# Optimization experiments

Measured on AMD Instinct MI355X. Metric: run time of the kernel, lower is better.

Reference implementation:

```python
import jax, jax.numpy as jnp
import numpy as np

PI = np.pi

def _rz(t):
    c, s = jnp.cos(t), jnp.sin(t)
    z, o = jnp.zeros_like(t), jnp.ones_like(t)
    return jnp.stack([jnp.stack([c, -s, z]), jnp.stack([s, c, z]), jnp.stack([z, z, o])])

def _ry(t):
    c, s = jnp.cos(t), jnp.sin(t)
    z, o = jnp.zeros_like(t), jnp.ones_like(t)
    return jnp.stack([jnp.stack([c, z, s]), jnp.stack([z, o, z]), jnp.stack([-s, z, c])])

def _zyz_affine(params, translate):
    # params: [6] in [0,1]; returns rotation matrix [3,3] and offset [3]
    phi   = params[0] * 2.0 * PI - PI
    theta = params[1] * 2.0 * PI - PI
    psi   = params[2] * 2.0 * PI - PI
    loc_r = params[3:6] * 2.0 - 1.0 if translate else params[3:6] * 0.0
    rm = (_rz(phi) @ _ry(theta) @ _rz(psi)).T
    c = -rm @ loc_r
    return rm, c

def _trilinear(img, x, y, z):
    # img: [X,Y,Z,C]; x,y,z: [X,Y,Z] normalized coords in [-1,1]
    xl, yl, zl, _ = img.shape
    x = (x + 1.0) * (xl - 1) * 0.5
    y = (y + 1.0) * (yl - 1) * 0.5
    z = (z + 1.0) * (zl - 1) * 0.5
    x0f, y0f, z0f = jnp.floor(x), jnp.floor(y), jnp.floor(z)
    x0 = jnp.clip(x0f.astype(jnp.int32), 0, xl - 1)
    x1 = jnp.clip(x0f.astype(jnp.int32) + 1, 0, xl - 1)
    y0 = jnp.clip(y0f.astype(jnp.int32), 0, yl - 1)
    y1 = jnp.clip(y0f.astype(jnp.int32) + 1, 0, yl - 1)
    z0 = jnp.clip(z0f.astype(jnp.int32), 0, zl - 1)
    z1 = jnp.clip(z0f.astype(jnp.int32) + 1, 0, zl - 1)
    # original computes dx against the *clipped* lower corner
    dx = (x - x0.astype(x.dtype))[..., None]
    dy = (y - y0.astype(y.dtype))[..., None]
    dz = (z - z0.astype(z.dtype))[..., None]
    out = ((1 - dx) * (1 - dy) * (1 - dz) * img[x0, y0, z0]
         + (1 - dx) * (1 - dy) * dz       * img[x0, y0, z1]
         + (1 - dx) * dy       * (1 - dz) * img[x0, y1, z0]
         + (1 - dx) * dy       * dz       * img[x0, y1, z1]
         + dx       * (1 - dy) * (1 - dz) * img[x1, y0, z0]
         + dx       * (1 - dy) * dz       * img[x1, y0, z1]
         + dx       * dy       * (1 - dz) * img[x1, y1, z0]
         + dx       * dy       * dz       * img[x1, y1, z1])
    return out

def _affine_warp(img, rm, c):
    xl, yl, zl = img.shape[:3]
    gx = jnp.linspace(-1.0, 1.0, xl)
    gy = jnp.linspace(-1.0, 1.0, yl)
    gz = jnp.linspace(-1.0, 1.0, zl)
    grids = jnp.stack(jnp.meshgrid(gx, gy, gz, indexing='ij'))  # [3,X,Y,Z]
    tg = jnp.einsum('ij,jxyz->ixyz', rm, grids) + c[:, None, None, None]
    return _trilinear(img, tg[0], tg[1], tg[2])

def _ft3d(x):
    # chain of three 1D FFTs + fftshift over spatial axes == fftshift(fftn)
    return jnp.fft.fftshift(jnp.fft.fftn(x.astype(jnp.complex64), axes=(1, 2, 3)), axes=(1, 2, 3))

def _ift3d(x):
    return jnp.fft.ifftn(jnp.fft.ifftshift(x, axes=(1, 2, 3)), axes=(1, 2, 3))

def setup_inputs() -> dict:
    key = jax.random.key(0)
    ks = jax.random.split(key, 5)
    B, N, C = 32, 64, 1
    return {
        'X': jax.random.normal(ks[0], (B, N, N, N, C), jnp.float32),
        'Y': jax.random.normal(ks[1], (B, N, N, N, C), jnp.float32),
        'm1': jax.random.uniform(ks[2], (B, N, N, N, C), jnp.float32),
        'm2': jax.random.uniform(ks[3], (B, N, N, N, C), jnp.float32),
        'theta': jax.random.uniform(ks[4], (B, 6), jnp.float32),
    }

def reference(X, Y, m1, m2, theta):
    # masks: rotation only (zero translation)
    mask_warp = jax.vmap(lambda m, p: _affine_warp(m, *_zyz_affine(p, False)))
    M1_t = mask_warp(m1, theta)
    M2_t = mask_warp(m2, theta)
    # 'fill' padding: rescale translations by shape/(shape+2), zero-pad, warp, crop
    shape = jnp.asarray(X.shape[1:4], jnp.float32)
    scale = jnp.concatenate([jnp.ones(3, jnp.float32), shape / (shape + 2.0)])
    theta_r = (theta - 0.5) * scale + 0.5
    Xp = jnp.pad(X, ((0, 0), (1, 1), (1, 1), (1, 1), (0, 0)))
    img_warp = jax.vmap(lambda im, p: _affine_warp(im, *_zyz_affine(p, True)))
    X_t = img_warp(Xp, theta_r)[:, 1:-1, 1:-1, 1:-1, :]
    fused = _ft3d(X_t) * M1_t.astype(jnp.complex64) + _ft3d(Y) * M2_t.astype(jnp.complex64)
    output = jnp.real(_ift3d(fused)).astype(jnp.float32)
    return output, M1_t, M2_t
```

## Files before the change

### kernel.cpp

```cpp
#include <hip/hip_runtime.h>
#include <math.h>

#define NB 32
#define NN 4096
#define NNN 262144
#define PERMI(i) ((((i)&7)<<3)|((i)>>3))

__device__ __forceinline__ float2 cadd(float2 a, float2 b){ return make_float2(a.x+b.x, a.y+b.y); }
__device__ __forceinline__ float2 csub(float2 a, float2 b){ return make_float2(a.x-b.x, a.y-b.y); }
__device__ __forceinline__ float2 cmulc(float2 a, float2 b){ return make_float2(a.x*b.x - a.y*b.y, a.x*b.y + a.y*b.x); }
template<int S> __device__ __forceinline__ float2 cmuli(float2 a){
  return (S>0)? make_float2(-a.y,a.x) : make_float2(a.y,-a.x);
}

template<int S>
__device__ __forceinline__ void dft8(float2* a){
  const float r_ = 0.70710678118654752f;
  float2 t0=cadd(a[0],a[4]), t1=csub(a[0],a[4]);
  float2 t2=cadd(a[2],a[6]), t3=csub(a[2],a[6]);
  float2 u0=cadd(a[1],a[5]), u1=csub(a[1],a[5]);
  float2 u2=cadd(a[3],a[7]), u3=csub(a[3],a[7]);
  float2 E0=cadd(t0,t2), E2=csub(t0,t2);
  float2 it3=cmuli<S>(t3);
  float2 E1=cadd(t1,it3), E3=csub(t1,it3);
  float2 O0=cadd(u0,u2), O2=csub(u0,u2);
  float2 iu3=cmuli<S>(u3);
  float2 O1=cadd(u1,iu3), O3=csub(u1,iu3);
  const float sr = (S>0)? r_ : -r_;
  float2 W1 = make_float2(r_, sr);
  float2 W3 = make_float2(-r_, sr);
  float2 o1 = cmulc(O1,W1);
  float2 o2 = cmuli<S>(O2);
  float2 o3 = cmulc(O3,W3);
  a[0]=cadd(E0,O0); a[4]=csub(E0,O0);
  a[1]=cadd(E1,o1); a[5]=csub(E1,o1);
  a[2]=cadd(E2,o2); a[6]=csub(E2,o2);
  a[3]=cadd(E3,o3); a[7]=csub(E3,o3);
}

#define TWTAB \
  const float TWC[8]={1.f,0.9951847266721969f,0.9807852804032304f,0.9569403357322088f, \
                      0.9238795325112867f,0.8819212643483551f,0.8314696123025452f,0.7730104533627370f}; \
  const float TWS[8]={0.f,0.0980171403295606f,0.1950903220161283f,0.2902846772544624f, \
                      0.3826834323650898f,0.4713967368259976f,0.5555702330196022f,0.6343932841636455f};

template<int S>
__device__ __forceinline__ void fft64(float2* v){
  #pragma unroll
  for(int n2=0;n2<8;n2++){
    float2 t[8];
    #pragma unroll
    for(int n1=0;n1<8;n1++) t[n1] = v[8*n1+n2];
    dft8<S>(t);
    #pragma unroll
    for(int k1=0;k1<8;k1++) v[8*k1+n2] = t[k1];
  }
  TWTAB
  #pragma unroll
  for(int k1=1;k1<8;k1++){
    float2 wb = make_float2(TWC[k1], (S>0)? TWS[k1] : -TWS[k1]);
    float2 w = wb;
    #pragma unroll
    for(int n2=1;n2<8;n2++){
      v[8*k1+n2] = cmulc(v[8*k1+n2], w);
      w = cmulc(w, wb);
    }
  }
  #pragma unroll
  for(int k1=0;k1<8;k1++){
    float2 t[8];
    #pragma unroll
    for(int n2=0;n2<8;n2++) t[n2]=v[8*k1+n2];
    dft8<S>(t);
    #pragma unroll
    for(int k2=0;k2<8;k2++) v[8*k1+k2]=t[k2];
  }
}

template<int S>
__device__ __forceinline__ void fft64_pin_nat(float2* v){
  #pragma unroll
  for(int r=0;r<8;r++){
    float2 t[8];
    #pragma unroll
    for(int a=0;a<8;a++) t[a]=v[8*r+a];
    dft8<S>(t);
    #pragma unroll
    for(int q=0;q<8;q++) v[8*r+q]=t[q];
  }
  TWTAB
  #pragma unroll
  for(int r=1;r<8;r++){
    float2 wb = make_float2(TWC[r], (S>0)? TWS[r] : -TWS[r]);
    float2 w = wb;
    #pragma unroll
    for(int q=1;q<8;q++){
      v[8*r+q] = cmulc(v[8*r+q], w);
      w = cmulc(w, wb);
    }
  }
  #pragma unroll
  for(int q=0;q<8;q++){
    float2 t[8];
    #pragma unroll
    for(int b=0;b<8;b++) t[b]=v[8*b+q];
    dft8<S>(t);
    #pragma unroll
    for(int m=0;m<8;m++) v[8*m+q]=t[m];
  }
}

__global__ void k_affine(const float* __restrict__ theta, float* __restrict__ aff){
  int b = threadIdx.x;
  if(b >= NB) return;
  const float* t = theta + b*6;
  const float PIf = 3.14159265358979323846f;
  float phi = t[0]*(2.f*PIf) - PIf;
  float th  = t[1]*(2.f*PIf) - PIf;
  float psi = t[2]*(2.f*PIf) - PIf;
  float cph = cosf(phi), sph = sinf(phi);
  float cth = cosf(th),  sth = sinf(th);
  float cps = cosf(psi), sps = sinf(psi);
  float R00 = cph*cth*cps - sph*sps;
  float R01 = -cph*cth*sps - sph*cps;
  float R02 = cph*sth;
  float R10 = sph*cth*cps + cph*sps;
  float R11 = -sph*cth*sps + cph*cps;
  float R12 = sph*sth;
  float R20 = -sth*cps;
  float R21 = sth*sps;
  float R22 = cth;
  float rm0=R00, rm1=R10, rm2=R20;
  float rm3=R01, rm4=R11, rm5=R21;
  float rm6=R02, rm7=R12, rm8=R22;
  float* o = aff + b*16;
  o[0]=rm0; o[1]=rm1; o[2]=rm2;
  o[3]=rm3; o[4]=rm4; o[5]=rm5;
  o[6]=rm6; o[7]=rm7; o[8]=rm8;
  const float sc = 64.0f/66.0f;
  float lx = (2.f*t[3]-1.f)*sc;
  float ly = (2.f*t[4]-1.f)*sc;
  float lz = (2.f*t[5]-1.f)*sc;
  o[9]  = -(rm0*lx + rm1*ly + rm2*lz);
  o[10] = -(rm3*lx + rm4*ly + rm5*lz);
  o[11] = -(rm6*lx + rm7*ly + rm8*lz);
}

__device__ __forceinline__ void tile_decode(int blk, int& batch, int& ox, int& oy, int& oz){
  int xcd = blk & 7;
  int j = blk >> 3;
  batch = xcd + ((j >> 9) << 3);
  int tile = j & 511;
  oz = (tile & 7) << 3;
  oy = ((tile >> 3) & 7) << 3;
  ox = (tile >> 6) << 3;
}

#define LDSI(xi,yi,zi) ((((xi)*16)+(yi))*17+(zi))

__global__ __launch_bounds__(256) void k_warp_masks(const float* __restrict__ m1, const float* __restrict__ m2,
                             const float* __restrict__ aff,
                             float* __restrict__ M1, float* __restrict__ M2){
  __shared__ float s1[16*16*17];
  __shared__ float s2[16*16*17];
  int batch, ox, oy, oz;
  tile_decode(blockIdx.x, batch, ox, oy, oz);
  const float* a = aff + batch*16;
  float a0=a[0],a1=a[1],a2=a[2],a3=a[3],a4=a[4],a5=a[5],a6=a[6],a7=a[7],a8=a[8];

  float gxl = ox*(2.f/63.f)-1.f, gxh = (ox+7)*(2.f/63.f)-1.f;
  float gyl = oy*(2.f/63.f)-1.f, gyh = (oy+7)*(2.f/63.f)-1.f;
  float gzl = oz*(2.f/63.f)-1.f, gzh = (oz+7)*(2.f/63.f)-1.f;
  #define MM(c,lo,hi) fminf((c)*(lo),(c)*(hi))
  float minx = (1.f + MM(a0,gxl,gxh) + MM(a1,gyl,gyh) + MM(a2,gzl,gzh))*31.5f;
  float miny = (1.f + MM(a3,gxl,gxh) + MM(a4,gyl,gyh) + MM(a5,gzl,gzh))*31.5f;
  float minz = (1.f + MM(a6,gxl,gxh) + MM(a7,gyl,gyh) + MM(a8,gzl,gzh))*31.5f;
  #undef MM
  int sx0 = min(max((int)floorf(minx-0.01f),0),48);
  int sy0 = min(max((int)floorf(miny-0.01f),0),48);
  int sz0 = min(max((int)floorf(minz-0.01f),0),48);

  {
    int zi = threadIdx.x & 15, yi = threadIdx.x >> 4;
    const float* p1 = m1 + (size_t)batch*NNN + ((sy0+yi)<<6) + (sz0+zi);
    const float* p2 = m2 + (size_t)batch*NNN + ((sy0+yi)<<6) + (sz0+zi);
    #pragma unroll
    for(int xi=0;xi<16;xi++){
      s1[LDSI(xi,yi,zi)] = p1[(size_t)(sx0+xi)<<12];
      s2[LDSI(xi,yi,zi)] = p2[(size_t)(sx0+xi)<<12];
    }
  }
  __syncthreads();

  #pragma unroll
  for(int o=0;o<2;o++){
    int v = threadIdx.x + o*256;
    int zo = v & 7, yo = (v>>3)&7, xo = v>>6;
    float gx = (ox+xo)*(2.f/63.f)-1.f;
    float gy = (oy+yo)*(2.f/63.f)-1.f;
    float gz = (oz+zo)*(2.f/63.f)-1.f;
    float px = (a0*gx + a1*gy + a2*gz + 1.f)*31.5f;
    float py = (a3*gx + a4*gy + a5*gz + 1.f)*31.5f;
    float pz = (a6*gx + a7*gy + a8*gz + 1.f)*31.5f;
    int xf=(int)floorf(px), yf=(int)floorf(py), zf=(int)floorf(pz);
    int x0=min(max(xf,0),63), x1=min(max(xf+1,0),63);
    int y0=min(max(yf,0),63), y1=min(max(yf+1,0),63);
    int z0=min(max(zf,0),63), z1=min(max(zf+1,0),63);
    float dx=px-(float)x0, dy=py-(float)y0, dz=pz-(float)z0;
    float ex=1.f-dx, ey=1.f-dy, ez=1.f-dz;
    int lx0=min(max(x0-sx0,0),15), lx1=min(max(x1-sx0,0),15);
    int ly0=min(max(y0-sy0,0),15), ly1=min(max(y1-sy0,0),15);
    int lz0=min(max(z0-sz0,0),15), lz1=min(max(z1-sz0,0),15);
    int xA=lx0*272, xB=lx1*272, yA=ly0*17, yB=ly1*17;
    int i000=xA+yA+lz0, i001=xA+yA+lz1, i010=xA+yB+lz0, i011=xA+yB+lz1;
    int i100=xB+yA+lz0, i101=xB+yA+lz1, i110=xB+yB+lz0, i111=xB+yB+lz1;
    float w000=ex*ey*ez, w001=ex*ey*dz, w010=ex*dy*ez, w011=ex*dy*dz;
    float w100=dx*ey*ez, w101=dx*ey*dz, w110=dx*dy*ez, w111=dx*dy*dz;
    float r1 = w000*s1[i000]+w001*s1[i001]+w010*s1[i010]+w011*s1[i011]
             + w100*s1[i100]+w101*s1[i101]+w110*s1[i110]+w111*s1[i111];
    float r2 = w000*s2[i000]+w001*s2[i001]+w010*s2[i010]+w011*s2[i011]
             + w100*s2[i100]+w101*s2[i101]+w110*s2[i110]+w111*s2[i111];
    size_t oi = (size_t)batch*NNN + ((size_t)(ox+xo)<<12) + ((oy+yo)<<6) + (oz+zo);
    M1[oi] = r1;
    M2[oi] = r2;
  }
}

__global__ __launch_bounds__(256) void k_warp_x(const float* __restrict__ X, const float* __restrict__ aff,
                         float* __restrict__ Xt){
  __shared__ float sX[16*16*17];
  int batch, ox, oy, oz;
  tile_decode(blockIdx.x, batch, ox, oy, oz);
  const float* a = aff + batch*16;
  float a0=a[0],a1=a[1],a2=a[2],a3=a[3],a4=a[4],a5=a[5],a6=a[6],a7=a[7],a8=a[8];
  float c0=a[9], c1=a[10], c2=a[11];

  float gxl = (ox+1)*(2.f/65.f)-1.f, gxh = (ox+8)*(2.f/65.f)-1.f;
  float gyl = (oy+1)*(2.f/65.f)-1.f, gyh = (oy+8)*(2.f/65.f)-1.f;
  float gzl = (oz+1)*(2.f/65.f)-1.f, gzh = (oz+8)*(2.f/65.f)-1.f;
  #define MM(c,lo,hi) fminf((c)*(lo),(c)*(hi))
  float minx = (MM(a0,gxl,gxh) + MM(a1,gyl,gyh) + MM(a2,gzl,gzh) + c0 + 1.f)*32.5f;
  float miny = (MM(a3,gxl,gxh) + MM(a4,gyl,gyh) + MM(a5,gzl,gzh) + c1 + 1.f)*32.5f;
  float minz = (MM(a6,gxl,gxh) + MM(a7,gyl,gyh) + MM(a8,gzl,gzh) + c2 + 1.f)*32.5f;
  #undef MM
  int sx0 = min(max((int)floorf(minx-0.01f),0),50);
  int sy0 = min(max((int)floorf(miny-0.01f),0),50);
  int sz0 = min(max((int)floorf(minz-0.01f),0),50);

  {
    int zi = threadIdx.x & 15, yi = threadIdx.x >> 4;
    int ys = sy0 + yi, zs = sz0 + zi;
    bool yz_ok = ((unsigned)(ys-1) < 64u) && ((unsigned)(zs-1) < 64u);
    const float* p = X + (size_t)batch*NNN + ((ys-1)<<6) + (zs-1);
    #pragma unroll
    for(int xi=0;xi<16;xi++){
      int xs = sx0 + xi;
      float val = (yz_ok && ((unsigned)(xs-1) < 64u)) ? p[(size_t)(xs-1)<<12] : 0.f;
      sX[LDSI(xi,yi,zi)] = val;
    }
  }
  __syncthreads();

  #pragma unroll
  for(int o=0;o<2;o++){
    int v = threadIdx.x + o*256;
    int zo = v & 7, yo = (v>>3)&7, xo = v>>6;
    float gx = (ox+xo+1)*(2.f/65.f)-1.f;
    float gy = (oy+yo+1)*(2.f/65.f)-1.f;
    float gz = (oz+zo+1)*(2.f/65.f)-1.f;
    float px = (a0*gx + a1*gy + a2*gz + c0 + 1.f)*32.5f;
    float py = (a3*gx + a4*gy + a5*gz + c1 + 1.f)*32.5f;
    float pz = (a6*gx + a7*gy + a8*gz + c2 + 1.f)*32.5f;
    int xf=(int)floorf(px), yf=(int)floorf(py), zf=(int)floorf(pz);
    int x0=min(max(xf,0),65), x1=min(max(xf+1,0),65);
    int y0=min(max(yf,0),65), y1=min(max(yf+1,0),65);
    int z0=min(max(zf,0),65), z1=min(max(zf+1,0),65);
    float dx=px-(float)x0, dy=py-(float)y0, dz=pz-(float)z0;
    float ex=1.f-dx, ey=1.f-dy, ez=1.f-dz;
    int lx0=min(max(x0-sx0,0),15), lx1=min(max(x1-sx0,0),15);
    int ly0=min(max(y0-sy0,0),15), ly1=min(max(y1-sy0,0),15);
    int lz0=min(max(z0-sz0,0),15), lz1=min(max(z1-sz0,0),15);
    int xA=lx0*272, xB=lx1*272, yA=ly0*17, yB=ly1*17;
    float rv = ex*ey*ez*sX[xA+yA+lz0] + ex*ey*dz*sX[xA+yA+lz1]
             + ex*dy*ez*sX[xA+yB+lz0] + ex*dy*dz*sX[xA+yB+lz1]
             + dx*ey*ez*sX[xB+yA+lz0] + dx*ey*dz*sX[xB+yA+lz1]
             + dx*dy*ez*sX[xB+yB+lz0] + dx*dy*dz*sX[xB+yB+lz1];
    size_t oi = (size_t)batch*NNN + ((size_t)(ox+xo)<<12) + ((oy+yo)<<6) + (oz+zo);
    Xt[oi] = rv;
  }
}

__global__ __launch_bounds__(64,1) void k_fwd_slab(const float* __restrict__ src, float2* __restrict__ dst){
  __shared__ float re[64*65];
  __shared__ float im[64*65];
  int s = blockIdx.x;
  int t = threadIdx.x;
  const float* p = src + (size_t)s*NN;
  float2 v[64];
  #pragma unroll
  for(int y=0;y<64;y++) v[y] = make_float2(p[y*64+t], 0.f);
  fft64<-1>(v);
  #pragma unroll
  for(int i=0;i<64;i++){ float2 q = v[PERMI(i)]; re[i*65+t]=q.x; im[i*65+t]=q.y; }
  __syncthreads();
  #pragma unroll
  for(int z=0;z<64;z++) v[z] = make_float2(re[t*65+z], im[t*65+z]);
  fft64<-1>(v);
  #pragma unroll
  for(int i=0;i<64;i++){ float2 q = v[PERMI(i)]; re[t*65+i]=q.x; im[t*65+i]=q.y; }
  __syncthreads();
  float2* d = dst + (size_t)s*NN;
  #pragma unroll
  for(int i=0;i<64;i++) d[i*64+t] = make_float2(re[i*65+t], im[i*65+t]);
}

__global__ __launch_bounds__(256,1) void k_conv_x(float2* __restrict__ A, const float* __restrict__ M){
  int lid = blockIdx.x*blockDim.x + threadIdx.x;
  int z = lid & 63, y = (lid>>6) & 63, b = lid>>12;
  float2* p = A + (size_t)b*NNN + y*64 + z;
  const float* m = M + (size_t)b*NNN + ((y^32)<<6) + (z^32);
  float2 v[64];
  #pragma unroll
  for(int k=0;k<64;k++) v[k] = p[(size_t)k*NN];
  fft64<-1>(v);
  #pragma unroll
  for(int i=0;i<64;i++){
    float mm = m[(size_t)(i^32)*NN];
    v[PERMI(i)].x *= mm;
    v[PERMI(i)].y *= mm;
  }
  fft64_pin_nat<1>(v);
  #pragma unroll
  for(int i=0;i<64;i++) p[(size_t)i*NN] = v[i];
}

template<bool ACC>
__global__ __launch_bounds__(64,1) void k_inv_slab(const float2* __restrict__ src, float* __restrict__ dst){
  __shared__ float re[64*65];
  __shared__ float im[64*65];
  int s = blockIdx.x;
  int t = threadIdx.x;
  const float2* p = src + (size_t)s*NN;
  float2 v[64];
  #pragma unroll
  for(int ky=0;ky<64;ky++) v[ky] = p[ky*64+t];
  fft64<1>(v);
  #pragma unroll
  for(int i=0;i<64;i++){ float2 q = v[PERMI(i)]; re[i*65+t]=q.x; im[i*65+t]=q.y; }
  __syncthreads();
  #pragma unroll
  for(int kz=0;kz<64;kz++) v[kz] = make_float2(re[t*65+kz], im[t*65+kz]);
  fft64<1>(v);
  const float scl = 1.0f/262144.0f;
  #pragma unroll
  for(int i=0;i<64;i++) re[t*65+i] = v[PERMI(i)].x * scl;
  __syncthreads();
  float* d = dst + (size_t)s*NN;
  #pragma unroll
  for(int i=0;i<64;i++){
    float val = re[i*65+t];
    if (ACC) d[i*64+t] += val; else d[i*64+t] = val;
  }
}

extern "C" void kernel_launch(void* const* d_in, const int* in_sizes, int n_in,
                              void* d_out, int out_size, void* d_ws, size_t ws_size,
                              hipStream_t stream){
  const float* X  = (const float*)d_in[0];
  const float* Y  = (const float*)d_in[1];
  const float* m1 = (const float*)d_in[2];
  const float* m2 = (const float*)d_in[3];
  const float* th = (const float*)d_in[4];
  float* out0 = (float*)d_out;
  float* out1 = out0 + (size_t)NB*NNN;
  float* out2 = out1 + (size_t)NB*NNN;
  float2* A  = (float2*)d_ws;
  float*  aff = (float*)((char*)d_ws + (size_t)NB*NNN*sizeof(float2));

  k_affine<<<dim3(1), dim3(32), 0, stream>>>(th, aff);
  k_warp_masks<<<dim3(NB*512), dim3(256), 0, stream>>>(m1, m2, aff, out1, out2);
  k_warp_x<<<dim3(NB*512), dim3(256), 0, stream>>>(X, aff, out0);

  k_fwd_slab<<<dim3(NB*64), dim3(64), 0, stream>>>(out0, A);
  k_conv_x<<<dim3(NB*NN/256), dim3(256), 0, stream>>>(A, out1);
  k_inv_slab<false><<<dim3(NB*64), dim3(64), 0, stream>>>(A, out0);

  k_fwd_slab<<<dim3(NB*64), dim3(64), 0, stream>>>(Y, A);
  k_conv_x<<<dim3(NB*NN/256), dim3(256), 0, stream>>>(A, out2);
  k_inv_slab<true><<<dim3(NB*64), dim3(64), 0, stream>>>(A, out0);
}
```

Before: 468.3 us.

## Store FFT intermediates and mask tiles in half precision and fuse inverse passes

Intermediate spectra in the workspace and the shared-memory transposes now use packed half2 instead of float2, and the two mask tiles are packed into one half2 LDS array. Scaling is split across stages (a 1/64 factor on the mask multiply) to keep values within fp16 range. The two inverse transforms become a single kernel that sums both spectra before the inverse FFT, which removes one inverse pass and the read-modify-write accumulate. The aim is to halve memory traffic. The cost is a large loss of precision in the FFT path and the warped masks, which risks exceeding the accuracy tolerance.

```diff
diff --git a/kernel.cpp b/kernel.cpp
--- a/kernel.cpp
+++ b/kernel.cpp
@@ -1,4 +1,5 @@
 #include <hip/hip_runtime.h>
+#include <hip/hip_fp16.h>
 #include <math.h>
 
 #define NB 32
@@ -109,6 +110,9 @@
     for(int m=0;m<8;m++) v[8*m+q]=t[m];
   }
 }
+
+__device__ __forceinline__ float2 h2f(__half2 h){ return __half22float2(h); }
+__device__ __forceinline__ __half2 f2h(float2 f){ return __floats2half2_rn(f.x, f.y); }
 
 __global__ void k_affine(const float* __restrict__ theta, float* __restrict__ aff){
   int b = threadIdx.x;
@@ -161,8 +165,7 @@
 __global__ __launch_bounds__(256) void k_warp_masks(const float* __restrict__ m1, const float* __restrict__ m2,
                              const float* __restrict__ aff,
                              float* __restrict__ M1, float* __restrict__ M2){
-  __shared__ float s1[16*16*17];
-  __shared__ float s2[16*16*17];
+  __shared__ __half2 s12[16*16*17];
   int batch, ox, oy, oz;
   tile_decode(blockIdx.x, batch, ox, oy, oz);
   const float* a = aff + batch*16;
@@ -186,8 +189,9 @@
     const float* p2 = m2 + (size_t)batch*NNN + ((sy0+yi)<<6) + (sz0+zi);
     #pragma unroll
     for(int xi=0;xi<16;xi++){
-      s1[LDSI(xi,yi,zi)] = p1[(size_t)(sx0+xi)<<12];
-      s2[LDSI(xi,yi,zi)] = p2[(size_t)(sx0+xi)<<12];
+      float f1 = p1[(size_t)(sx0+xi)<<12];
+      float f2 = p2[(size_t)(sx0+xi)<<12];
+      s12[LDSI(xi,yi,zi)] = __floats2half2_rn(f1, f2);
     }
   }
   __syncthreads();
@@ -212,14 +216,16 @@
     int ly0=min(max(y0-sy0,0),15), ly1=min(max(y1-sy0,0),15);
     int lz0=min(max(z0-sz0,0),15), lz1=min(max(z1-sz0,0),15);
     int xA=lx0*272, xB=lx1*272, yA=ly0*17, yB=ly1*17;
-    int i000=xA+yA+lz0, i001=xA+yA+lz1, i010=xA+yB+lz0, i011=xA+yB+lz1;
-    int i100=xB+yA+lz0, i101=xB+yA+lz1, i110=xB+yB+lz0, i111=xB+yB+lz1;
+    float2 c000=h2f(s12[xA+yA+lz0]), c001=h2f(s12[xA+yA+lz1]);
+    float2 c010=h2f(s12[xA+yB+lz0]), c011=h2f(s12[xA+yB+lz1]);
+    float2 c100=h2f(s12[xB+yA+lz0]), c101=h2f(s12[xB+yA+lz1]);
+    float2 c110=h2f(s12[xB+yB+lz0]), c111=h2f(s12[xB+yB+lz1]);
     float w000=ex*ey*ez, w001=ex*ey*dz, w010=ex*dy*ez, w011=ex*dy*dz;
     float w100=dx*ey*ez, w101=dx*ey*dz, w110=dx*dy*ez, w111=dx*dy*dz;
-    float r1 = w000*s1[i000]+w001*s1[i001]+w010*s1[i010]+w011*s1[i011]
-             + w100*s1[i100]+w101*s1[i101]+w110*s1[i110]+w111*s1[i111];
-    float r2 = w000*s2[i000]+w001*s2[i001]+w010*s2[i010]+w011*s2[i011]
-             + w100*s2[i100]+w101*s2[i101]+w110*s2[i110]+w111*s2[i111];
+    float r1 = w000*c000.x+w001*c001.x+w010*c010.x+w011*c011.x
+             + w100*c100.x+w101*c101.x+w110*c110.x+w111*c111.x;
+    float r2 = w000*c000.y+w001*c001.y+w010*c010.y+w011*c011.y
+             + w100*c100.y+w101*c101.y+w110*c110.y+w111*c111.y;
     size_t oi = (size_t)batch*NNN + ((size_t)(ox+xo)<<12) + ((oy+yo)<<6) + (oz+zo);
     M1[oi] = r1;
     M2[oi] = r2;
@@ -290,9 +296,8 @@
   }
 }
 
-__global__ __launch_bounds__(64,1) void k_fwd_slab(const float* __restrict__ src, float2* __restrict__ dst){
-  __shared__ float re[64*65];
-  __shared__ float im[64*65];
+__global__ __launch_bounds__(64,1) void k_fwd_slab(const float* __restrict__ src, __half2* __restrict__ dst){
+  __shared__ __half2 sh[64*65];
   int s = blockIdx.x;
   int t = threadIdx.x;
   const float* p = src + (size_t)s*NN;
@@ -301,66 +306,71 @@
   for(int y=0;y<64;y++) v[y] = make_float2(p[y*64+t], 0.f);
   fft64<-1>(v);
   #pragma unroll
-  for(int i=0;i<64;i++){ float2 q = v[PERMI(i)]; re[i*65+t]=q.x; im[i*65+t]=q.y; }
-  __syncthreads();
-  #pragma unroll
-  for(int z=0;z<64;z++) v[z] = make_float2(re[t*65+z], im[t*65+z]);
+  for(int i=0;i<64;i++) sh[i*65+t] = f2h(v[PERMI(i)]);
+  __syncthreads();
+  #pragma unroll
+  for(int z=0;z<64;z++) v[z] = h2f(sh[t*65+z]);
   fft64<-1>(v);
-  #pragma unroll
-  for(int i=0;i<64;i++){ float2 q = v[PERMI(i)]; re[t*65+i]=q.x; im[t*65+i]=q.y; }
-  __syncthreads();
-  float2* d = dst + (size_t)s*NN;
-  #pragma unroll
-  for(int i=0;i<64;i++) d[i*64+t] = make_float2(re[i*65+t], im[i*65+t]);
-}
-
-__global__ __launch_bounds__(256,1) void k_conv_x(float2* __restrict__ A, const float* __restrict__ M){
+  __syncthreads();
+  #pragma unroll
+  for(int i=0;i<64;i++) sh[t*65+i] = f2h(v[PERMI(i)]);
+  __syncthreads();
+  __half2* d = dst + (size_t)s*NN;
+  #pragma unroll
+  for(int i=0;i<64;i++) d[i*64+t] = sh[i*65+t];
+}
+
+__global__ __launch_bounds__(256,1) void k_conv_x(__half2* __restrict__ A, const float* __restrict__ M){
   int lid = blockIdx.x*blockDim.x + threadIdx.x;
   int z = lid & 63, y = (lid>>6) & 63, b = lid>>12;
-  float2* p = A + (size_t)b*NNN + y*64 + z;
+  __half2* p = A + (size_t)b*NNN + y*64 + z;
   const float* m = M + (size_t)b*NNN + ((y^32)<<6) + (z^32);
   float2 v[64];
   #pragma unroll
-  for(int k=0;k<64;k++) v[k] = p[(size_t)k*NN];
+  for(int k=0;k<64;k++) v[k] = h2f(p[(size_t)k*NN]);
   fft64<-1>(v);
   #pragma unroll
   for(int i=0;i<64;i++){
-    float mm = m[(size_t)(i^32)*NN];
+    float mm = m[(size_t)(i^32)*NN] * 0.015625f;
     v[PERMI(i)].x *= mm;
     v[PERMI(i)].y *= mm;
   }
   fft64_pin_nat<1>(v);
   #pragma unroll
-  for(int i=0;i<64;i++) p[(size_t)i*NN] = v[i];
-}
-
-template<bool ACC>
-__global__ __launch_bounds__(64,1) void k_inv_slab(const float2* __restrict__ src, float* __restrict__ dst){
-  __shared__ float re[64*65];
-  __shared__ float im[64*65];
+  for(int i=0;i<64;i++) p[(size_t)i*NN] = f2h(v[i]);
+}
+
+__global__ __launch_bounds__(64,1) void k_inv_sum(const __half2* __restrict__ a,
+                                                  const __half2* __restrict__ bb,
+                                                  float* __restrict__ dst){
+  __shared__ float sre[64*65];
+  __half2* shh = (__half2*)sre;
   int s = blockIdx.x;
   int t = threadIdx.x;
-  const float2* p = src + (size_t)s*NN;
+  const __half2* pa = a  + (size_t)s*NN;
+  const __half2* pb = bb + (size_t)s*NN;
   float2 v[64];
   #pragma unroll
-  for(int ky=0;ky<64;ky++) v[ky] = p[ky*64+t];
+  for(int ky=0;ky<64;ky++){
+    float2 fa = h2f(pa[ky*64+t]);
+    float2 fb = h2f(pb[ky*64+t]);
+    v[ky] = cadd(fa, fb);
+  }
   fft64<1>(v);
   #pragma unroll
-  for(int i=0;i<64;i++){ float2 q = v[PERMI(i)]; re[i*65+t]=q.x; im[i*65+t]=q.y; }
-  __syncthreads();
-  #pragma unroll
-  for(int kz=0;kz<64;kz++) v[kz] = make_float2(re[t*65+kz], im[t*65+kz]);
+  for(int i=0;i<64;i++) shh[i*65+t] = f2h(v[PERMI(i)]);
+  __syncthreads();
+  #pragma unroll
+  for(int kz=0;kz<64;kz++) v[kz] = h2f(shh[t*65+kz]);
+  __syncthreads();
   fft64<1>(v);
-  const float scl = 1.0f/262144.0f;
-  #pragma unroll
-  for(int i=0;i<64;i++) re[t*65+i] = v[PERMI(i)].x * scl;
+  const float scl = 1.0f/4096.0f;
+  #pragma unroll
+  for(int i=0;i<64;i++) sre[t*65+i] = v[PERMI(i)].x * scl;
   __syncthreads();
   float* d = dst + (size_t)s*NN;
   #pragma unroll
-  for(int i=0;i<64;i++){
-    float val = re[i*65+t];
-    if (ACC) d[i*64+t] += val; else d[i*64+t] = val;
-  }
+  for(int i=0;i<64;i++) d[i*64+t] = sre[i*65+t];
 }
 
 extern "C" void kernel_launch(void* const* d_in, const int* in_sizes, int n_in,
@@ -374,8 +384,9 @@
   float* out0 = (float*)d_out;
   float* out1 = out0 + (size_t)NB*NNN;
   float* out2 = out1 + (size_t)NB*NNN;
-  float2* A  = (float2*)d_ws;
-  float*  aff = (float*)((char*)d_ws + (size_t)NB*NNN*sizeof(float2));
+  __half2* A = (__half2*)d_ws;
+  __half2* B = A + (size_t)NB*NNN;
+  float*  aff = (float*)((char*)d_ws + 2*(size_t)NB*NNN*sizeof(__half2));
 
   k_affine<<<dim3(1), dim3(32), 0, stream>>>(th, aff);
   k_warp_masks<<<dim3(NB*512), dim3(256), 0, stream>>>(m1, m2, aff, out1, out2);
@@ -383,9 +394,7 @@
 
   k_fwd_slab<<<dim3(NB*64), dim3(64), 0, stream>>>(out0, A);
   k_conv_x<<<dim3(NB*NN/256), dim3(256), 0, stream>>>(A, out1);
-  k_inv_slab<false><<<dim3(NB*64), dim3(64), 0, stream>>>(A, out0);
-
-  k_fwd_slab<<<dim3(NB*64), dim3(64), 0, stream>>>(Y, A);
-  k_conv_x<<<dim3(NB*NN/256), dim3(256), 0, stream>>>(A, out2);
-  k_inv_slab<true><<<dim3(NB*64), dim3(64), 0, stream>>>(A, out0);
-}
+  k_fwd_slab<<<dim3(NB*64), dim3(64), 0, stream>>>(Y, B);
+  k_conv_x<<<dim3(NB*NN/256), dim3(256), 0, stream>>>(B, out2);
+  k_inv_sum<<<dim3(NB*64), dim3(64), 0, stream>>>(A, B, out0);
+}
```

After: 422.5 us. -9.8%, faster.
